# Kernel optimization log

Hardware: AMD Instinct MI355X
Metric: run time of the kernel (lower is better)

Reference implementation:

```python
import jax, jax.numpy as jnp
import numpy as np

N, P, C = 100000, 48, 8
D, H = 64, 4
DH = D // H
FLAG = 7
EPS = 1e-5


def _layer_norm(x, g, b):
    mu = x.mean(-1, keepdims=True)
    var = ((x - mu) ** 2).mean(-1, keepdims=True)
    return (x - mu) * jax.lax.rsqrt(var + EPS) * g + b


def setup_inputs() -> dict:
    key = jax.random.key(0)
    ks = jax.random.split(key, 24)
    w = lambda k, shp: (jax.random.normal(k, shp, dtype=jnp.float32) * 0.05)
    inp = {
        "voxel_features": jax.random.normal(ks[0], (N, D), dtype=jnp.float32),
        "voxels": jax.random.normal(ks[1], (N, P, C), dtype=jnp.float32),
        "pp_w1": w(ks[2], (D, C)), "pp_b1": w(ks[3], (D,)),
        "pp_w2": w(ks[4], (D, D)), "pp_b2": w(ks[5], (D,)),
        "in_proj_w": w(ks[6], (3 * D, D)), "in_proj_b": w(ks[7], (3 * D,)),
        "out_w": w(ks[8], (D, D)), "out_b": w(ks[9], (D,)),
        "ln1_g": jnp.ones((D,), jnp.float32), "ln1_b": jnp.zeros((D,), jnp.float32),
        "ffn_w1": w(ks[10], (2 * D, D)), "ffn_b1": w(ks[11], (2 * D,)),
        "ffn_w2": w(ks[12], (D, 2 * D)), "ffn_b2": w(ks[13], (D,)),
        "ln2_g": jnp.ones((D,), jnp.float32), "ln2_b": jnp.zeros((D,), jnp.float32),
        "op_w1": w(ks[14], (D, D)), "op_b1": w(ks[15], (D,)),
        "op_w2": w(ks[16], (D, D)), "op_b2": w(ks[17], (D,)),
        "num_points": jax.random.randint(ks[18], (N,), 0, P, dtype=jnp.int32),
    }
    return inp


def reference(voxel_features, voxels, pp_w1, pp_b1, pp_w2, pp_b2,
              in_proj_w, in_proj_b, out_w, out_b, ln1_g, ln1_b,
              ffn_w1, ffn_b1, ffn_w2, ffn_b2, ln2_g, ln2_b,
              op_w1, op_b1, op_w2, op_b2, num_points):
    n, p, _ = voxels.shape
    point_mask = jnp.arange(p)[None, :] < num_points[:, None]          # [N,P]
    current_mask = (voxels[:, :, FLAG] > 0.5) & point_mask             # [N,P]
    history_mask = point_mask & ~current_mask                          # [N,P]
    history_present = history_mask.any(axis=1, keepdims=True)          # [N,1]

    point_features = voxels[:, :, :C]

    def masked_mean(vals, mask):
        m = mask.astype(vals.dtype)[..., None]
        counts = jnp.clip(mask.sum(1, keepdims=True), 1, None).astype(vals.dtype)
        return (vals * m).sum(1) / counts                              # [N,C]

    cur_sum = masked_mean(point_features, current_mask)
    his_sum = masked_mean(point_features, history_mask)

    def point_proj(x):
        return jax.nn.relu(x @ pp_w1.T + pp_b1) @ pp_w2.T + pp_b2

    tokens = jnp.stack([voxel_features, point_proj(cur_sum), point_proj(his_sum)], axis=1)  # [N,3,D]

    key_pad = jnp.stack([jnp.zeros((n,), bool),
                         ~current_mask.any(1),
                         ~history_present[:, 0]], axis=1)              # [N,3]

    # multi-head self-attention over 3 tokens
    qkv = tokens @ in_proj_w.T + in_proj_b                             # [N,3,3D]
    q, k, v = jnp.split(qkv, 3, axis=-1)
    q = q.reshape(n, 3, H, DH).transpose(0, 2, 1, 3)                   # [N,H,3,DH]
    k = k.reshape(n, 3, H, DH).transpose(0, 2, 1, 3)
    v = v.reshape(n, 3, H, DH).transpose(0, 2, 1, 3)
    scores = jnp.einsum('nhqd,nhkd->nhqk', q, k) / np.sqrt(DH)
    scores = jnp.where(key_pad[:, None, None, :], -jnp.inf, scores)
    attn = jax.nn.softmax(scores, axis=-1)
    ctx = jnp.einsum('nhqk,nhkd->nhqd', attn, v)                       # [N,H,3,DH]
    ctx = ctx.transpose(0, 2, 1, 3).reshape(n, 3, D)
    attn_out = ctx @ out_w.T + out_b

    tokens = _layer_norm(tokens + attn_out, ln1_g, ln1_b)
    ffn = jax.nn.relu(tokens @ ffn_w1.T + ffn_b1) @ ffn_w2.T + ffn_b2
    tokens = _layer_norm(tokens + ffn, ln2_g, ln2_b)

    refined = jax.nn.relu(tokens[:, 0] @ op_w1.T + op_b1) @ op_w2.T + op_b2
    refined = refined * history_present.astype(refined.dtype)
    return voxel_features + refined
```

## Files before the change

kernel.cpp:

```cpp
#include <hip/hip_runtime.h>


using bf16x8 = __attribute__((ext_vector_type(8))) __bf16;
using f32x4  = __attribute__((ext_vector_type(4))) float;

#define DEV static __device__ __forceinline__

DEV float bf2f(unsigned short u){
  union { unsigned int i; float f; } v; v.i = ((unsigned int)u) << 16; return v.f;
}
DEV unsigned short f2bf(float f){
  union { float f; unsigned int i; } v; v.f = f;
  unsigned int x = v.i;
  x += 0x7FFFu + ((x >> 16) & 1u);
  return (unsigned short)(x >> 16);
}

DEV unsigned short* lp(unsigned short* base, int row, int col){
  int byte = (col << 1) ^ ((row & 7) << 4);
  return (unsigned short*)((char*)base + (row << 7) + byte);
}

DEV bf16x8 ldA(const unsigned short* base, int mt, int kt, int lane){
  int row = mt*16 + (lane & 15);
  int col = kt*32 + ((lane >> 4) << 3);
  return *(const bf16x8*)lp((unsigned short*)base, row, col);
}
DEV bf16x8 ldB(const unsigned short* w, int frag, int lane){
  return *(const bf16x8*)(w + (size_t)frag*512 + (size_t)lane*8);
}
DEV void stC(unsigned short* base, int mt, int nt, f32x4 c, int lane){
  int col  = nt*16 + (lane & 15);
  int row0 = mt*16 + ((lane >> 4) << 2);
  #pragma unroll
  for (int r = 0; r < 4; ++r) *lp(base, row0 + r, col) = f2bf(c[r]);
}
DEV f32x4 MF(bf16x8 a, bf16x8 b, f32x4 c){
  return __builtin_amdgcn_mfma_f32_16x16x32_bf16(a, b, c, 0, 0, 0);
}

DEV void ld16(const unsigned short* base, int row, int col0, float* o){
  uint4 a = *(const uint4*)lp((unsigned short*)base, row, col0);
  uint4 b = *(const uint4*)lp((unsigned short*)base, row, col0 + 8);
  unsigned int w[8] = {a.x, a.y, a.z, a.w, b.x, b.y, b.z, b.w};
  #pragma unroll
  for (int i = 0; i < 8; ++i){
    union { unsigned int u; float f; } lo, hi;
    lo.u = w[i] << 16; hi.u = w[i] & 0xFFFF0000u;
    o[2*i] = lo.f; o[2*i+1] = hi.f;
  }
}
DEV void st16(unsigned short* base, int row, int col0, const float* f){
  unsigned int w[8];
  #pragma unroll
  for (int i = 0; i < 8; ++i)
    w[i] = (unsigned int)f2bf(f[2*i]) | ((unsigned int)f2bf(f[2*i+1]) << 16);
  *(uint4*)lp(base, row, col0)     = make_uint4(w[0], w[1], w[2], w[3]);
  *(uint4*)lp(base, row, col0 + 8) = make_uint4(w[4], w[5], w[6], w[7]);
}

DEV bf16x8 pack8(const float* f){
  union { bf16x8 v; unsigned short u[8]; } r;
  #pragma unroll
  for (int i = 0; i < 8; ++i) r.u[i] = f2bf(f[i]);
  return r.v;
}

DEV void layer_norm16(f32x4 x[4], const float* g, const float* b, int lane){
  float s[4], s2[4];
  #pragma unroll
  for (int r = 0; r < 4; ++r){
    s[r]  = x[0][r] + x[1][r] + x[2][r] + x[3][r];
    s2[r] = x[0][r]*x[0][r] + x[1][r]*x[1][r] + x[2][r]*x[2][r] + x[3][r]*x[3][r];
  }
  #pragma unroll
  for (int o = 1; o <= 8; o <<= 1){
    #pragma unroll
    for (int r = 0; r < 4; ++r){
      s[r]  += __shfl_xor(s[r],  o);
      s2[r] += __shfl_xor(s2[r], o);
    }
  }
  float mu[4], rs[4];
  #pragma unroll
  for (int r = 0; r < 4; ++r){
    mu[r] = s[r] * (1.f/64.f);
    float var = s2[r] * (1.f/64.f) - mu[r]*mu[r];
    rs[r] = rsqrtf(var + 1e-5f);
  }
  const int cl = lane & 15;
  #pragma unroll
  for (int nt = 0; nt < 4; ++nt){
    float gg = g[nt*16 + cl], bb = b[nt*16 + cl];
    #pragma unroll
    for (int r = 0; r < 4; ++r)
      x[nt][r] = (x[nt][r] - mu[r]) * rs[r] * gg + bb;
  }
}

__global__ void tva_pack_weights(const float* __restrict__ pp_w1, const float* __restrict__ pp_w2,
                                 const float* __restrict__ in_proj_w, const float* __restrict__ out_w,
                                 const float* __restrict__ ffn_w1, const float* __restrict__ ffn_w2,
                                 const float* __restrict__ op_w1, const float* __restrict__ op_w2,
                                 unsigned short* __restrict__ ws)
{
  int b = blockIdx.x, lane = threadIdx.x;
  const float* W; int base, ktiles, K;
  if      (b < 4)  { W = pp_w1;     base = 0;  ktiles = 1; K = 8;   }
  else if (b < 12) { W = pp_w2;     base = 4;  ktiles = 2; K = 64;  }
  else if (b < 36) { W = in_proj_w; base = 12; ktiles = 2; K = 64;  }
  else if (b < 44) { W = out_w;     base = 36; ktiles = 2; K = 64;  }
  else if (b < 60) { W = ffn_w1;    base = 44; ktiles = 2; K = 64;  }
  else if (b < 76) { W = ffn_w2;    base = 60; ktiles = 4; K = 128; }
  else if (b < 84) { W = op_w1;     base = 76; ktiles = 2; K = 64;  }
  else             { W = op_w2;     base = 84; ktiles = 2; K = 64;  }
  int local = b - base;
  int nt = local / ktiles, kt = local % ktiles;
  int n  = nt*16 + (lane & 15);
  int k0 = kt*32 + ((lane >> 4) << 3);
  unsigned short* dst = ws + (size_t)b*512 + (size_t)lane*8;
  #pragma unroll
  for (int i = 0; i < 8; ++i){
    int k = k0 + i;
    float v = (k < K) ? W[(size_t)n*K + k] : 0.0f;
    dst[i] = f2bf(v);
  }
}

__global__ __launch_bounds__(128)
void tva_main(const float* __restrict__ vf, const float* __restrict__ vox,
              const int* __restrict__ num_points,
              const float* __restrict__ pp_b1, const float* __restrict__ pp_b2,
              const float* __restrict__ ipb,  const float* __restrict__ outb,
              const float* __restrict__ ln1g, const float* __restrict__ ln1b,
              const float* __restrict__ f1b,  const float* __restrict__ f2bv,
              const float* __restrict__ ln2g, const float* __restrict__ ln2b,
              const float* __restrict__ o1b,  const float* __restrict__ o2b,
              const unsigned short* __restrict__ wfrag,
              float* __restrict__ out, int nvox)
{
  __shared__ unsigned short smem[2 * 64 * 64];
  const int tid  = threadIdx.x;
  const int wv   = tid >> 6;
  const int lane = tid & 63;
  unsigned short* X = smem + wv * (64*64);
  unsigned short* Q = X + 48*64;

  const int v0 = (blockIdx.x * 2 + wv) * 16;
  if (v0 >= nvox) return;
  const int cl = lane & 15;
  const int r0 = (lane >> 4) << 2;

  const int vi = lane >> 2, pq = lane & 3;
  const int np = num_points[v0 + vi];
  float cs[8] = {0,0,0,0,0,0,0,0}, hs[8] = {0,0,0,0,0,0,0,0};
  float cc = 0.f, hc = 0.f;
  const float4* vp = (const float4*)(vox + (size_t)(v0 + vi) * 384);
  #pragma unroll
  for (int k = 0; k < 12; ++k){
    int p = pq + (k << 2);
    float4 a = vp[p*2], b = vp[p*2 + 1];
    float pm = (p < np) ? 1.f : 0.f;
    float cm = (b.w > 0.5f) ? pm : 0.f;
    float hm = pm - cm;
    cc += cm; hc += hm;
    cs[0] += a.x*cm; cs[1] += a.y*cm; cs[2] += a.z*cm; cs[3] += a.w*cm;
    cs[4] += b.x*cm; cs[5] += b.y*cm; cs[6] += b.z*cm; cs[7] += b.w*cm;
    hs[0] += a.x*hm; hs[1] += a.y*hm; hs[2] += a.z*hm; hs[3] += a.w*hm;
    hs[4] += b.x*hm; hs[5] += b.y*hm; hs[6] += b.z*hm; hs[7] += b.w*hm;
  }
  #pragma unroll
  for (int o = 1; o <= 2; o <<= 1){
    cc += __shfl_xor(cc, o); hc += __shfl_xor(hc, o);
    #pragma unroll
    for (int j = 0; j < 8; ++j){
      cs[j] += __shfl_xor(cs[j], o);
      hs[j] += __shfl_xor(hs[j], o);
    }
  }
  const float icc = 1.f / fmaxf(cc, 1.f);
  const float ihc = 1.f / fmaxf(hc, 1.f);
  const unsigned int myfw = (cc > 0.f ? 1u : 0u) | (hc > 0.f ? 2u : 0u);

  bf16x8 ac, ah;
  {
    const int src = cl * 4;
    float cf[8], hf[8];
    #pragma unroll
    for (int i = 0; i < 8; ++i){
      cf[i] = __shfl(cs[i]*icc, src);
      hf[i] = __shfl(hs[i]*ihc, src);
    }
    union { bf16x8 v; unsigned short u[8]; } rc, rh;
    #pragma unroll
    for (int i = 0; i < 8; ++i){
      rc.u[i] = (lane < 16) ? f2bf(cf[i]) : (unsigned short)0;
      rh.u[i] = (lane < 16) ? f2bf(hf[i]) : (unsigned short)0;
    }
    ac = rc.v; ah = rh.v;
  }

  #pragma unroll
  for (int nt = 0; nt < 4; ++nt){
    float bb = pp_b1[nt*16 + cl];
    f32x4 c0 = {bb, bb, bb, bb}, c1 = {bb, bb, bb, bb};
    bf16x8 B = ldB(wfrag, nt, lane);
    c0 = MF(ac, B, c0);
    c1 = MF(ah, B, c1);
    #pragma unroll
    for (int r = 0; r < 4; ++r){ c0[r] = fmaxf(c0[r], 0.f); c1[r] = fmaxf(c1[r], 0.f); }
    stC(X, 0, nt, c0, lane);
    stC(X, 1, nt, c1, lane);
  }
  {
    bf16x8 hfr[2][2];
    #pragma unroll
    for (int m = 0; m < 2; ++m)
      #pragma unroll
      for (int kt = 0; kt < 2; ++kt) hfr[m][kt] = ldA(X, m, kt, lane);
    #pragma unroll
    for (int m = 0; m < 2; ++m){
      #pragma unroll
      for (int nt = 0; nt < 4; ++nt){
        float bb = pp_b2[nt*16 + cl];
        f32x4 c = {bb, bb, bb, bb};
        c = MF(hfr[m][0], ldB(wfrag, 4 + nt*2 + 0, lane), c);
        c = MF(hfr[m][1], ldB(wfrag, 4 + nt*2 + 1, lane), c);
        stC(X, m, nt, c, lane);
      }
    }
  }

  bf16x8 at[3][2];
  {
    const float* s = vf + (size_t)(v0 + cl) * 64 + ((lane >> 4) << 3);
    #pragma unroll
    for (int kt = 0; kt < 2; ++kt){
      float4 x0 = *(const float4*)(s + kt*32);
      float4 x1 = *(const float4*)(s + kt*32 + 4);
      float f[8] = {x0.x, x0.y, x0.z, x0.w, x1.x, x1.y, x1.z, x1.w};
      at[0][kt] = pack8(f);
    }
    #pragma unroll
    for (int kt = 0; kt < 2; ++kt){
      at[1][kt] = ldA(X, 0, kt, lane);
      at[2][kt] = ldA(X, 1, kt, lane);
    }
  }
  #pragma unroll
  for (int nt = 0; nt < 4; ++nt){
    float bb = ipb[nt*16 + cl];
    f32x4 c = {bb, bb, bb, bb};
    c = MF(at[0][0], ldB(wfrag, 12 + nt*2 + 0, lane), c);
    c = MF(at[0][1], ldB(wfrag, 12 + nt*2 + 1, lane), c);
    #pragma unroll
    for (int r = 0; r < 4; ++r) c[r] *= 0.25f;
    stC(Q, 0, nt, c, lane);
  }
  #pragma unroll
  for (int m = 0; m < 3; ++m){
    #pragma unroll
    for (int nt = 0; nt < 4; ++nt){
      int ntg = 4 + nt;
      float bb = ipb[64 + nt*16 + cl];
      f32x4 c = {bb, bb, bb, bb};
      c = MF(at[m][0], ldB(wfrag, 12 + ntg*2 + 0, lane), c);
      c = MF(at[m][1], ldB(wfrag, 12 + ntg*2 + 1, lane), c);
      stC(X, m, nt, c, lane);
    }
  }

  const int av = cl, hh2 = lane >> 4;
  float p0, p1, p2;
  {
    unsigned int fw = (unsigned int)__shfl((int)myfw, av*4);
    bool caZ = (fw & 1u) != 0, hpZ = (fw & 2u) != 0;
    float q[16]; ld16(Q, av, hh2*16, q);
    float sc[3];
    #pragma unroll
    for (int m = 0; m < 3; ++m){
      float kv[16]; ld16(X, m*16 + av, hh2*16, kv);
      float d = 0.f;
      #pragma unroll
      for (int j = 0; j < 16; ++j) d += q[j]*kv[j];
      sc[m] = d;
    }
    float mx = sc[0];
    mx = caZ ? fmaxf(mx, sc[1]) : mx;
    mx = hpZ ? fmaxf(mx, sc[2]) : mx;
    p0 = __expf(sc[0] - mx);
    p1 = caZ ? __expf(sc[1] - mx) : 0.f;
    p2 = hpZ ? __expf(sc[2] - mx) : 0.f;
    float inv = 1.f / (p0 + p1 + p2);
    p0 *= inv; p1 *= inv; p2 *= inv;
  }

  #pragma unroll
  for (int m = 0; m < 3; ++m){
    #pragma unroll
    for (int nt = 0; nt < 4; ++nt){
      int ntg = 8 + nt;
      float bb = ipb[128 + nt*16 + cl];
      f32x4 c = {bb, bb, bb, bb};
      c = MF(at[m][0], ldB(wfrag, 12 + ntg*2 + 0, lane), c);
      c = MF(at[m][1], ldB(wfrag, 12 + ntg*2 + 1, lane), c);
      stC(X, m, nt, c, lane);
    }
  }

  {
    float ctx[16];
    float vv[16];
    ld16(X, av, hh2*16, vv);
    #pragma unroll
    for (int j = 0; j < 16; ++j) ctx[j] = p0*vv[j];
    ld16(X, 16 + av, hh2*16, vv);
    #pragma unroll
    for (int j = 0; j < 16; ++j) ctx[j] += p1*vv[j];
    ld16(X, 32 + av, hh2*16, vv);
    #pragma unroll
    for (int j = 0; j < 16; ++j) ctx[j] += p2*vv[j];
    st16(Q, av, hh2*16, ctx);
  }

  f32x4 res1[4];
  {
    bf16x8 a0 = ldA(Q, 0, 0, lane), a1 = ldA(Q, 0, 1, lane);
    float rv[16];
    #pragma unroll
    for (int nt = 0; nt < 4; ++nt)
      #pragma unroll
      for (int r = 0; r < 4; ++r)
        rv[nt*4 + r] = vf[(size_t)(v0 + r0 + r)*64 + nt*16 + cl];
    #pragma unroll
    for (int nt = 0; nt < 4; ++nt){
      float bb = outb[nt*16 + cl];
      f32x4 c = {bb, bb, bb, bb};
      c = MF(a0, ldB(wfrag, 36 + nt*2 + 0, lane), c);
      c = MF(a1, ldB(wfrag, 36 + nt*2 + 1, lane), c);
      #pragma unroll
      for (int r = 0; r < 4; ++r) c[r] += rv[nt*4 + r];
      res1[nt] = c;
    }
    layer_norm16(res1, ln1g, ln1b, lane);
    #pragma unroll
    for (int nt = 0; nt < 4; ++nt) stC(Q, 0, nt, res1[nt], lane);
  }

  f32x4 tk2[4];
  {
    bf16x8 a0 = ldA(Q, 0, 0, lane), a1 = ldA(Q, 0, 1, lane);
    #pragma unroll
    for (int nt = 0; nt < 4; ++nt){
      float bb = f2bv[nt*16 + cl];
      tk2[nt] = (f32x4){bb, bb, bb, bb};
    }
    #pragma unroll
    for (int nt = 0; nt < 4; ++nt){
      float bb = f1b[nt*16 + cl];
      f32x4 c = {bb, bb, bb, bb};
      c = MF(a0, ldB(wfrag, 44 + nt*2 + 0, lane), c);
      c = MF(a1, ldB(wfrag, 44 + nt*2 + 1, lane), c);
      #pragma unroll
      for (int r = 0; r < 4; ++r) c[r] = fmaxf(c[r], 0.f);
      stC(X, 0, nt, c, lane);
    }
    {
      bf16x8 h0 = ldA(X, 0, 0, lane), h1 = ldA(X, 0, 1, lane);
      #pragma unroll
      for (int nt = 0; nt < 4; ++nt){
        tk2[nt] = MF(h0, ldB(wfrag, 60 + nt*4 + 0, lane), tk2[nt]);
        tk2[nt] = MF(h1, ldB(wfrag, 60 + nt*4 + 1, lane), tk2[nt]);
      }
    }
    #pragma unroll
    for (int nt = 4; nt < 8; ++nt){
      float bb = f1b[nt*16 + cl];
      f32x4 c = {bb, bb, bb, bb};
      c = MF(a0, ldB(wfrag, 44 + nt*2 + 0, lane), c);
      c = MF(a1, ldB(wfrag, 44 + nt*2 + 1, lane), c);
      #pragma unroll
      for (int r = 0; r < 4; ++r) c[r] = fmaxf(c[r], 0.f);
      stC(X, 0, nt - 4, c, lane);
    }
    {
      bf16x8 h0 = ldA(X, 0, 0, lane), h1 = ldA(X, 0, 1, lane);
      #pragma unroll
      for (int nt = 0; nt < 4; ++nt){
        tk2[nt] = MF(h0, ldB(wfrag, 60 + nt*4 + 2, lane), tk2[nt]);
        tk2[nt] = MF(h1, ldB(wfrag, 60 + nt*4 + 3, lane), tk2[nt]);
      }
    }
    #pragma unroll
    for (int nt = 0; nt < 4; ++nt)
      #pragma unroll
      for (int r = 0; r < 4; ++r) tk2[nt][r] += res1[nt][r];
    layer_norm16(tk2, ln2g, ln2b, lane);
    #pragma unroll
    for (int nt = 0; nt < 4; ++nt) stC(Q, 0, nt, tk2[nt], lane);
  }

  {
    bf16x8 a0 = ldA(Q, 0, 0, lane), a1 = ldA(Q, 0, 1, lane);
    #pragma unroll
    for (int nt = 0; nt < 4; ++nt){
      float bb = o1b[nt*16 + cl];
      f32x4 c = {bb, bb, bb, bb};
      c = MF(a0, ldB(wfrag, 76 + nt*2 + 0, lane), c);
      c = MF(a1, ldB(wfrag, 76 + nt*2 + 1, lane), c);
      #pragma unroll
      for (int r = 0; r < 4; ++r) c[r] = fmaxf(c[r], 0.f);
      stC(X, 0, nt, c, lane);
    }
    bf16x8 b0 = ldA(X, 0, 0, lane), b1 = ldA(X, 0, 1, lane);
    #pragma unroll
    for (int nt = 0; nt < 4; ++nt){
      float bb = o2b[nt*16 + cl];
      f32x4 c = {bb, bb, bb, bb};
      c = MF(b0, ldB(wfrag, 84 + nt*2 + 0, lane), c);
      c = MF(b1, ldB(wfrag, 84 + nt*2 + 1, lane), c);
      #pragma unroll
      for (int r = 0; r < 4; ++r){
        int row = r0 + r;
        unsigned int fw2 = (unsigned int)__shfl((int)myfw, row*4);
        float keep = (fw2 & 2u) ? 1.f : 0.f;
        size_t idx = (size_t)(v0 + row)*64 + nt*16 + cl;
        out[idx] = vf[idx] + keep * c[r];
      }
    }
  }
}

extern "C" void kernel_launch(void* const* d_in, const int* in_sizes, int n_in,
                              void* d_out, int out_size, void* d_ws, size_t ws_size,
                              hipStream_t stream)
{
  (void)n_in; (void)out_size; (void)ws_size;
  const float* vf    = (const float*)d_in[0];
  const float* vox   = (const float*)d_in[1];
  const float* pp_w1 = (const float*)d_in[2];
  const float* pp_b1 = (const float*)d_in[3];
  const float* pp_w2 = (const float*)d_in[4];
  const float* pp_b2 = (const float*)d_in[5];
  const float* ipw   = (const float*)d_in[6];
  const float* ipb   = (const float*)d_in[7];
  const float* outw  = (const float*)d_in[8];
  const float* outb  = (const float*)d_in[9];
  const float* ln1g  = (const float*)d_in[10];
  const float* ln1b  = (const float*)d_in[11];
  const float* f1w   = (const float*)d_in[12];
  const float* f1b   = (const float*)d_in[13];
  const float* f2w   = (const float*)d_in[14];
  const float* f2b   = (const float*)d_in[15];
  const float* ln2g  = (const float*)d_in[16];
  const float* ln2b  = (const float*)d_in[17];
  const float* o1w   = (const float*)d_in[18];
  const float* o1b   = (const float*)d_in[19];
  const float* o2w   = (const float*)d_in[20];
  const float* o2b   = (const float*)d_in[21];
  const int*   npts  = (const int*)d_in[22];
  unsigned short* wfrag = (unsigned short*)d_ws;
  float* out = (float*)d_out;

  const int nvox = in_sizes[0] / 64;
  const int ngrp = nvox / 16;
  const int nblk = (ngrp + 1) / 2;
  tva_pack_weights<<<92, 64, 0, stream>>>(pp_w1, pp_w2, ipw, outw, f1w, f2w, o1w, o2w, wfrag);
  tva_main<<<nblk, 128, 0, stream>>>(vf, vox, npts, pp_b1, pp_b2, ipb, outb,
                                     ln1g, ln1b, f1b, f2b, ln2g, ln2b, o1b, o2b,
                                     wfrag, out, nvox);
}
```

Before: 72.24 us.

## Disable unrolling of MFMA tile loops, hoist weight loads and keep-mask shuffles

Several MFMA loops over output tiles now use unroll 1 to cut register pressure. The weight fragment loads are hoisted out of the per-row-tile loop so each fragment is loaded once and reused across token tiles. The keep-mask shuffles in the epilogue are hoisted out of the tile loop, and float-to-bf16 conversion drops round-to-nearest-even tie handling for plain round-half-up. Not unrolling may expose load latency and add loop overhead in exchange for higher occupancy, and the rounding change can alter low bits of results.

```diff
diff --git a/kernel.cpp b/kernel.cpp
--- a/kernel.cpp
+++ b/kernel.cpp
@@ -6,14 +6,9 @@
 
 #define DEV static __device__ __forceinline__
 
-DEV float bf2f(unsigned short u){
-  union { unsigned int i; float f; } v; v.i = ((unsigned int)u) << 16; return v.f;
-}
 DEV unsigned short f2bf(float f){
   union { float f; unsigned int i; } v; v.f = f;
-  unsigned int x = v.i;
-  x += 0x7FFFu + ((x >> 16) & 1u);
-  return (unsigned short)(x >> 16);
+  return (unsigned short)((v.i + 0x8000u) >> 16);
 }
 
 DEV unsigned short* lp(unsigned short* base, int row, int col){
@@ -200,7 +195,7 @@
     ac = rc.v; ah = rh.v;
   }
 
-  #pragma unroll
+  #pragma unroll 1
   for (int nt = 0; nt < 4; ++nt){
     float bb = pp_b1[nt*16 + cl];
     f32x4 c0 = {bb, bb, bb, bb}, c1 = {bb, bb, bb, bb};
@@ -218,14 +213,16 @@
     for (int m = 0; m < 2; ++m)
       #pragma unroll
       for (int kt = 0; kt < 2; ++kt) hfr[m][kt] = ldA(X, m, kt, lane);
-    #pragma unroll
-    for (int m = 0; m < 2; ++m){
-      #pragma unroll
-      for (int nt = 0; nt < 4; ++nt){
-        float bb = pp_b2[nt*16 + cl];
+    #pragma unroll 1
+    for (int nt = 0; nt < 4; ++nt){
+      float bb = pp_b2[nt*16 + cl];
+      bf16x8 W0 = ldB(wfrag, 4 + nt*2 + 0, lane);
+      bf16x8 W1 = ldB(wfrag, 4 + nt*2 + 1, lane);
+      #pragma unroll
+      for (int m = 0; m < 2; ++m){
         f32x4 c = {bb, bb, bb, bb};
-        c = MF(hfr[m][0], ldB(wfrag, 4 + nt*2 + 0, lane), c);
-        c = MF(hfr[m][1], ldB(wfrag, 4 + nt*2 + 1, lane), c);
+        c = MF(hfr[m][0], W0, c);
+        c = MF(hfr[m][1], W1, c);
         stC(X, m, nt, c, lane);
       }
     }
@@ -247,7 +244,7 @@
       at[2][kt] = ldA(X, 1, kt, lane);
     }
   }
-  #pragma unroll
+  #pragma unroll 1
   for (int nt = 0; nt < 4; ++nt){
     float bb = ipb[nt*16 + cl];
     f32x4 c = {bb, bb, bb, bb};
@@ -257,15 +254,17 @@
     for (int r = 0; r < 4; ++r) c[r] *= 0.25f;
     stC(Q, 0, nt, c, lane);
   }
-  #pragma unroll
-  for (int m = 0; m < 3; ++m){
-    #pragma unroll
-    for (int nt = 0; nt < 4; ++nt){
-      int ntg = 4 + nt;
-      float bb = ipb[64 + nt*16 + cl];
-      f32x4 c = {bb, bb, bb, bb};
-      c = MF(at[m][0], ldB(wfrag, 12 + ntg*2 + 0, lane), c);
-      c = MF(at[m][1], ldB(wfrag, 12 + ntg*2 + 1, lane), c);
+  #pragma unroll 1
+  for (int nt = 0; nt < 4; ++nt){
+    int ntg = 4 + nt;
+    float bb = ipb[64 + nt*16 + cl];
+    bf16x8 W0 = ldB(wfrag, 12 + ntg*2 + 0, lane);
+    bf16x8 W1 = ldB(wfrag, 12 + ntg*2 + 1, lane);
+    #pragma unroll
+    for (int m = 0; m < 3; ++m){
+      f32x4 c = {bb, bb, bb, bb};
+      c = MF(at[m][0], W0, c);
+      c = MF(at[m][1], W1, c);
       stC(X, m, nt, c, lane);
     }
   }
@@ -295,15 +294,17 @@
     p0 *= inv; p1 *= inv; p2 *= inv;
   }
 
-  #pragma unroll
-  for (int m = 0; m < 3; ++m){
-    #pragma unroll
-    for (int nt = 0; nt < 4; ++nt){
-      int ntg = 8 + nt;
-      float bb = ipb[128 + nt*16 + cl];
-      f32x4 c = {bb, bb, bb, bb};
-      c = MF(at[m][0], ldB(wfrag, 12 + ntg*2 + 0, lane), c);
-      c = MF(at[m][1], ldB(wfrag, 12 + ntg*2 + 1, lane), c);
+  #pragma unroll 1
+  for (int nt = 0; nt < 4; ++nt){
+    int ntg = 8 + nt;
+    float bb = ipb[128 + nt*16 + cl];
+    bf16x8 W0 = ldB(wfrag, 12 + ntg*2 + 0, lane);
+    bf16x8 W1 = ldB(wfrag, 12 + ntg*2 + 1, lane);
+    #pragma unroll
+    for (int m = 0; m < 3; ++m){
+      f32x4 c = {bb, bb, bb, bb};
+      c = MF(at[m][0], W0, c);
+      c = MF(at[m][1], W1, c);
       stC(X, m, nt, c, lane);
     }
   }
@@ -355,7 +356,7 @@
       float bb = f2bv[nt*16 + cl];
       tk2[nt] = (f32x4){bb, bb, bb, bb};
     }
-    #pragma unroll
+    #pragma unroll 1
     for (int nt = 0; nt < 4; ++nt){
       float bb = f1b[nt*16 + cl];
       f32x4 c = {bb, bb, bb, bb};
@@ -373,7 +374,7 @@
         tk2[nt] = MF(h1, ldB(wfrag, 60 + nt*4 + 1, lane), tk2[nt]);
       }
     }
-    #pragma unroll
+    #pragma unroll 1
     for (int nt = 4; nt < 8; ++nt){
       float bb = f1b[nt*16 + cl];
       f32x4 c = {bb, bb, bb, bb};
@@ -402,7 +403,7 @@
 
   {
     bf16x8 a0 = ldA(Q, 0, 0, lane), a1 = ldA(Q, 0, 1, lane);
-    #pragma unroll
+    #pragma unroll 1
     for (int nt = 0; nt < 4; ++nt){
       float bb = o1b[nt*16 + cl];
       f32x4 c = {bb, bb, bb, bb};
@@ -413,7 +414,13 @@
       stC(X, 0, nt, c, lane);
     }
     bf16x8 b0 = ldA(X, 0, 0, lane), b1 = ldA(X, 0, 1, lane);
-    #pragma unroll
+    float keep[4];
+    #pragma unroll
+    for (int r = 0; r < 4; ++r){
+      unsigned int fw2 = (unsigned int)__shfl((int)myfw, (r0 + r)*4);
+      keep[r] = (fw2 & 2u) ? 1.f : 0.f;
+    }
+    #pragma unroll 1
     for (int nt = 0; nt < 4; ++nt){
       float bb = o2b[nt*16 + cl];
       f32x4 c = {bb, bb, bb, bb};
@@ -421,11 +428,8 @@
       c = MF(b1, ldB(wfrag, 84 + nt*2 + 1, lane), c);
       #pragma unroll
       for (int r = 0; r < 4; ++r){
-        int row = r0 + r;
-        unsigned int fw2 = (unsigned int)__shfl((int)myfw, row*4);
-        float keep = (fw2 & 2u) ? 1.f : 0.f;
-        size_t idx = (size_t)(v0 + row)*64 + nt*16 + cl;
-        out[idx] = vf[idx] + keep * c[r];
+        size_t idx = (size_t)(v0 + r0 + r)*64 + nt*16 + cl;
+        out[idx] = vf[idx] + keep[r] * c[r];
       }
     }
   }
```

After: 78.95 us. 9.3% more time.
